# Kernel optimization log

Hardware: AMD Instinct MI355X
Metric: run time of the kernel (lower is better)

## Reference

```python
import jax, jax.numpy as jnp
import numpy as np

B, T, I, H, C, L, N_AHEAD = 64, 512, 64, 512, 512, 2, 24


def _lstm_layer(x, w_ih, w_hh, b_ih, b_hh):
    """PyTorch-convention LSTM layer. x: [B,T,in]. Returns (outputs [B,T,H], hT, cT)."""
    bsz = x.shape[0]
    hdim = w_hh.shape[1]
    bias = b_ih + b_hh

    def step(carry, xt):
        h, c = carry
        g = xt @ w_ih.T + h @ w_hh.T + bias  # [B, 4H], gate order i,f,g,o
        i, f, gg, o = jnp.split(g, 4, axis=-1)
        c = jax.nn.sigmoid(f) * c + jax.nn.sigmoid(i) * jnp.tanh(gg)
        h = jax.nn.sigmoid(o) * jnp.tanh(c)
        return (h, c), h

    init = (jnp.zeros((bsz, hdim), x.dtype), jnp.zeros((bsz, hdim), x.dtype))
    (hT, cT), hs = jax.lax.scan(step, init, jnp.swapaxes(x, 0, 1))
    return jnp.swapaxes(hs, 0, 1), hT, cT


def setup_inputs() -> dict:
    key = jax.random.key(0)
    ks = jax.random.split(key, 16)
    s = 0.04  # ~ 1/sqrt(H) init scale
    d = {
        "x": jax.random.normal(ks[0], (B, T, I), jnp.float32),
        "w_ih0": jax.random.normal(ks[1], (4 * H, I), jnp.float32) * s,
        "w_hh0": jax.random.normal(ks[2], (4 * H, H), jnp.float32) * s,
        "b_ih0": jax.random.normal(ks[3], (4 * H,), jnp.float32) * s,
        "b_hh0": jax.random.normal(ks[4], (4 * H,), jnp.float32) * s,
        "w_ih1": jax.random.normal(ks[5], (4 * H, H), jnp.float32) * s,
        "w_hh1": jax.random.normal(ks[6], (4 * H, H), jnp.float32) * s,
        "b_ih1": jax.random.normal(ks[7], (4 * H,), jnp.float32) * s,
        "b_hh1": jax.random.normal(ks[8], (4 * H,), jnp.float32) * s,
        "w_ih_dec": jax.random.normal(ks[9], (4 * H, C), jnp.float32) * s,
        "w_hh_dec": jax.random.normal(ks[10], (4 * H, H), jnp.float32) * s,
        "b_ih_dec": jax.random.normal(ks[11], (4 * H,), jnp.float32) * s,
        "b_hh_dec": jax.random.normal(ks[12], (4 * H,), jnp.float32) * s,
        "w_fc": jax.random.normal(ks[13], (C, H), jnp.float32) * s,
        "b_fc": jax.random.normal(ks[14], (C,), jnp.float32) * s,
    }
    return d


def reference(x, w_ih0, w_hh0, b_ih0, b_hh0, w_ih1, w_hh1, b_ih1, b_hh1,
              w_ih_dec, w_hh_dec, b_ih_dec, b_hh_dec, w_fc, b_fc):
    # ---- encoder: 2-layer LSTM, batch_first ----
    h0_out, _, _ = _lstm_layer(x, w_ih0, w_hh0, b_ih0, b_hh0)
    enc, hT, cT = _lstm_layer(h0_out, w_ih1, w_hh1, b_ih1, b_hh1)  # enc: [B,T,H]

    bsz = x.shape[0]
    dec_bias = b_ih_dec + b_hh_dec
    dec_in0 = jnp.zeros((bsz, C), x.dtype)

    def dec_step(carry, _):
        h, c, dec_in = carry
        aw = jax.nn.softmax(jnp.einsum('bth,bh->bt', enc, h), axis=1)  # [B,T]
        ctx = jnp.einsum('bt,bth->bh', aw, enc)                         # [B,H]
        xi = dec_in + ctx                                               # requires C == H
        g = xi @ w_ih_dec.T + h @ w_hh_dec.T + dec_bias
        i, f, gg, o = jnp.split(g, 4, axis=-1)
        c = jax.nn.sigmoid(f) * c + jax.nn.sigmoid(i) * jnp.tanh(gg)
        h = jax.nn.sigmoid(o) * jnp.tanh(c)
        pred = h @ w_fc.T + b_fc                                        # [B,C]
        return (h, c, pred), pred

    _, preds = jax.lax.scan(dec_step, (hT, cT, dec_in0), None, length=N_AHEAD)
    return jnp.swapaxes(preds, 0, 1)  # [B, n_ahead, C]
```

## Files before the change

### kernel.cpp

```cpp
#include <hip/hip_runtime.h>

#define BATCH  64
#define TT     512
#define IDIM   64
#define HDIM   512
#define NAHEAD 24
#define HB     (HDIM * BATCH)

#define WIH0_OFF   0
#define WHH0_OFF   512
#define WIH1_OFF   4608
#define WHH1_OFF   8704
#define SCR_OFF    12800
#define GL_OFF     30208
#define BIAS_OFF   31232
#define ENC_SMEM_FLOATS 31248
#define ENC_SMEM_BYTES  (ENC_SMEM_FLOATS * 4)

typedef float v2f __attribute__((ext_vector_type(2)));

__device__ __forceinline__ float4 ld4(const float* p) {
  return *reinterpret_cast<const float4*>(p);
}
__device__ __forceinline__ float sigm(float x) { return 1.0f / (1.0f + expf(-x)); }

__device__ __forceinline__ void flag_barrier(unsigned* flags, unsigned* release,
                                             unsigned epoch, int bid) {
  asm volatile("s_waitcnt vmcnt(0)" ::: "memory");
  __syncthreads();
  if (threadIdx.x == 0)
    __hip_atomic_store(&flags[(size_t)bid * 16], epoch,
                       __ATOMIC_RELAXED, __HIP_MEMORY_SCOPE_AGENT);
  asm volatile("" ::: "memory");
  if (bid == 0 && threadIdx.x < 64) {
    const int l = threadIdx.x;
    for (;;) {
      bool ok = true;
#pragma unroll
      for (int i = 0; i < 4; ++i) {
        unsigned v = __hip_atomic_load(&flags[(size_t)(l * 4 + i) * 16],
                                       __ATOMIC_RELAXED, __HIP_MEMORY_SCOPE_AGENT);
        ok &= (v >= epoch);
      }
      if (__all(ok)) break;
      __builtin_amdgcn_s_sleep(1);
    }
    if (threadIdx.x == 0)
      __hip_atomic_store(release, epoch, __ATOMIC_RELAXED,
                         __HIP_MEMORY_SCOPE_AGENT);
  }
  if (threadIdx.x == 0) {
    while (__hip_atomic_load(release, __ATOMIC_RELAXED,
                             __HIP_MEMORY_SCOPE_AGENT) < epoch)
      __builtin_amdgcn_s_sleep(1);
  }
  __syncthreads();
  asm volatile("" ::: "memory");
}

#define STG8(dst, base, off0)                                          \
  _Pragma("unroll") for (int i = 0; i < 8; ++i) {                      \
    dst[i].x = (base)[((off0) + i) * BATCH];                           \
    dst[i].y = (base)[((off0) + i) * BATCH + 32];                      \
  }

#define BURN_S(sarr, C0)                                                      \
  do {                                                                        \
    _Pragma("unroll") for (int c = 0; c < 8; c += 4) {                        \
      if (t < TT) {                                                           \
        _Pragma("unroll") for (int d = 0; d < 8; ++d) {                       \
          float4 w = ld4(&smem[WHH0_OFF + d * HDIM + ks * 16 + (C0) + c]);    \
          a0[d] += sarr[c]*w.x + sarr[c+1]*w.y + sarr[c+2]*w.z + sarr[c+3]*w.w;\
        }                                                                     \
      }                                                                       \
      if (t >= 1) {                                                           \
        _Pragma("unroll") for (int d = 0; d < 8; ++d) {                       \
          float4 w = ld4(&smem[WIH1_OFF + d * HDIM + ks * 16 + (C0) + c]);    \
          a1[d] += sarr[c]*w.x + sarr[c+1]*w.y + sarr[c+2]*w.z + sarr[c+3]*w.w;\
        }                                                                     \
      }                                                                       \
    }                                                                         \
  } while (0)

#define BURN_E(earr, C0)                                                      \
  do {                                                                        \
    if (t >= 1) {                                                             \
      _Pragma("unroll") for (int c = 0; c < 8; c += 4) {                      \
        _Pragma("unroll") for (int d = 0; d < 8; ++d) {                       \
          float4 w = ld4(&smem[WHH1_OFF + d * HDIM + ks * 16 + (C0) + c]);    \
          a1[d] += earr[c]*w.x + earr[c+1]*w.y + earr[c+2]*w.z + earr[c+3]*w.w;\
        }                                                                     \
      }                                                                       \
    }                                                                         \
  } while (0)

__global__ __launch_bounds__(1024, 4)
void encoder_coop(const float* __restrict__ xT,
                  const float* __restrict__ w_ih0, const float* __restrict__ w_hh0,
                  const float* __restrict__ b_ih0, const float* __restrict__ b_hh0,
                  const float* __restrict__ w_ih1, const float* __restrict__ w_hh1,
                  const float* __restrict__ b_ih1, const float* __restrict__ b_hh1,
                  float* __restrict__ seq0,
                  float* __restrict__ enc,
                  float* __restrict__ cst1,
                  unsigned* flags, unsigned* release)
{
  extern __shared__ float smem[];
  const int tid  = threadIdx.x;
  const int bid  = blockIdx.x;
  const int j0   = bid * 2;
  const int lane = tid & 63;
  const int wv   = tid >> 6;
  const int bp   = tid & 31;
  const int ks   = tid >> 5;

  for (int idx = tid; idx < 8 * IDIM; idx += 1024) {
    int d = idx >> 6, k = idx & 63;
    size_t r = (size_t)((d >> 1) * HDIM + j0 + (d & 1));
    smem[WIH0_OFF + idx] = w_ih0[r * IDIM + k];
  }
  for (int idx = tid; idx < 8 * HDIM; idx += 1024) {
    int d = idx >> 9, k = idx & 511;
    size_t r = (size_t)((d >> 1) * HDIM + j0 + (d & 1));
    smem[WHH0_OFF + idx] = w_hh0[r * HDIM + k];
    smem[WIH1_OFF + idx] = w_ih1[r * HDIM + k];
    smem[WHH1_OFF + idx] = w_hh1[r * HDIM + k];
  }
  if (tid < 16) {
    int d = tid & 7;
    size_t r = (size_t)((d >> 1) * HDIM + j0 + (d & 1));
    smem[BIAS_OFF + tid] = (tid < 8) ? (b_ih0[r] + b_hh0[r])
                                     : (b_ih1[r] + b_hh1[r]);
  }
  __syncthreads();

  float c0 = 0.f;
  float c1 = 0.f;

  for (int t = 0; t <= TT; ++t) {
    const float* sp = seq0 + (size_t)t * HB + (size_t)(ks * 16) * BATCH + bp;
    const float* ep = enc + (size_t)(t >= 1 ? t - 1 : 0) * HB
                          + (size_t)(ks * 16) * BATCH + bp;

    v2f sA[8], sB[8], eA[8], eB[8];
    v2f xv[4];

    STG8(sA, sp, 0);
    STG8(sB, sp, 8);
    if (t < TT && ks < 16) {
      const float* xp = xT + (size_t)t * IDIM * BATCH
                           + (size_t)(ks * 4) * BATCH + bp;
#pragma unroll
      for (int i = 0; i < 4; ++i) {
        xv[i].x = xp[i * BATCH];
        xv[i].y = xp[i * BATCH + 32];
      }
    }

    v2f a0[8], a1[8];
#pragma unroll
    for (int d = 0; d < 8; ++d) { a0[d] = 0.f; a1[d] = 0.f; }

    if (t < TT && ks < 16) {
#pragma unroll
      for (int d = 0; d < 8; ++d) {
        float4 w = ld4(&smem[WIH0_OFF + d * IDIM + ks * 4]);
        a0[d] += xv[0]*w.x + xv[1]*w.y + xv[2]*w.z + xv[3]*w.w;
      }
    }

    BURN_S(sA, 0);
    if (t >= 1) STG8(eA, ep, 0);
    BURN_S(sB, 8);
    if (t >= 1) STG8(eB, ep, 8);
    BURN_E(eA, 0);
    BURN_E(eB, 8);

#pragma unroll
    for (int d = 0; d < 8; ++d) {
      float m0x = a0[d].x + __shfl_xor(a0[d].x, 32);
      float m0y = a0[d].y + __shfl_xor(a0[d].y, 32);
      smem[SCR_OFF + (d * 64 + lane) * 17 + wv] = (lane >= 32) ? m0y : m0x;
      float m1x = a1[d].x + __shfl_xor(a1[d].x, 32);
      float m1y = a1[d].y + __shfl_xor(a1[d].y, 32);
      smem[SCR_OFF + ((8 + d) * 64 + lane) * 17 + wv] = (lane >= 32) ? m1y : m1x;
    }
    __syncthreads();

    {
      const int dd = tid >> 6, bb = tid & 63;
      float s = 0.f;
#pragma unroll
      for (int i = 0; i < 16; ++i) s += smem[SCR_OFF + (dd * 64 + bb) * 17 + i];
      smem[GL_OFF + dd * 64 + bb] = s + smem[BIAS_OFF + dd];
    }
    __syncthreads();

    if (tid < 256) {
      const int bb = tid & 63, u = tid >> 6;
      if (u < 2) {
        if (t < TT) {
          const int cl = u;
          float gi = smem[GL_OFF + (0 + cl) * 64 + bb];
          float gf = smem[GL_OFF + (2 + cl) * 64 + bb];
          float gg = smem[GL_OFF + (4 + cl) * 64 + bb];
          float go = smem[GL_OFF + (6 + cl) * 64 + bb];
          float cn = sigm(gf) * c0 + sigm(gi) * tanhf(gg);
          float hn = sigm(go) * tanhf(cn);
          c0 = cn;
          __hip_atomic_store(
              &seq0[(size_t)(t + 1) * HB + (size_t)(j0 + cl) * BATCH + bb],
              hn, __ATOMIC_RELAXED, __HIP_MEMORY_SCOPE_AGENT);
        }
      } else {
        if (t >= 1) {
          const int cl = u - 2;
          float gi = smem[GL_OFF + (8 + 0 + cl) * 64 + bb];
          float gf = smem[GL_OFF + (8 + 2 + cl) * 64 + bb];
          float gg = smem[GL_OFF + (8 + 4 + cl) * 64 + bb];
          float go = smem[GL_OFF + (8 + 6 + cl) * 64 + bb];
          float cn = sigm(gf) * c1 + sigm(gi) * tanhf(gg);
          float hn = sigm(go) * tanhf(cn);
          c1 = cn;
          __hip_atomic_store(
              &enc[(size_t)t * HB + (size_t)(j0 + cl) * BATCH + bb],
              hn, __ATOMIC_RELAXED, __HIP_MEMORY_SCOPE_AGENT);
        }
      }
    }

    if (t < TT) flag_barrier(flags, release, (unsigned)(t + 1), bid);
  }

  if (tid >= 128 && tid < 256)
    cst1[(size_t)(j0 + ((tid >> 6) - 2)) * BATCH + (tid & 63)] = c1;
}

template <int DIN0>
__device__ __forceinline__ void cell_tile2(
    int j0, const float* __restrict__ in0,
    const float* __restrict__ h_in,
    const float* __restrict__ w_ih,
    const float* __restrict__ w_hh,
    const float* __restrict__ b_ih, const float* __restrict__ b_hh,
    float* __restrict__ c_state,
    float* __restrict__ h_out,
    float* __restrict__ sm)
{
  const int tid = threadIdx.x;
  const int b  = tid & 63;
  const int ks = tid >> 6;
  constexpr int K  = DIN0 + HDIM;
  constexpr int KS = K / 16;
  const int k0 = ks * KS, k1 = k0 + KS;
  const int a0 = (k0 < DIN0) ? k0 : DIN0;
  const int a1 = (k1 < DIN0) ? k1 : DIN0;
  const int c0 = (k0 > DIN0) ? k0 - DIN0 : 0;
  const int c1 = (k1 > DIN0) ? k1 - DIN0 : 0;

  const float* wi = w_ih + (size_t)j0 * DIN0;
  const float* wh = w_hh + (size_t)j0 * HDIM;

  float acc[8] = {0.f, 0.f, 0.f, 0.f, 0.f, 0.f, 0.f, 0.f};

#pragma unroll 2
  for (int k = a0; k < a1; k += 4) {
    float x0 = in0[(k + 0) * BATCH + b];
    float x1 = in0[(k + 1) * BATCH + b];
    float x2 = in0[(k + 2) * BATCH + b];
    float x3 = in0[(k + 3) * BATCH + b];
#pragma unroll
    for (int d = 0; d < 8; ++d) {
      float4 w = ld4(wi + (size_t)((d >> 1) * HDIM + (d & 1)) * DIN0 + k);
      acc[d] += x0 * w.x + x1 * w.y + x2 * w.z + x3 * w.w;
    }
  }
#pragma unroll 2
  for (int k = c0; k < c1; k += 4) {
    float h0 = h_in[(k + 0) * BATCH + b];
    float h1 = h_in[(k + 1) * BATCH + b];
    float h2 = h_in[(k + 2) * BATCH + b];
    float h3 = h_in[(k + 3) * BATCH + b];
#pragma unroll
    for (int d = 0; d < 8; ++d) {
      float4 w = ld4(wh + (size_t)((d >> 1) * HDIM + (d & 1)) * HDIM + k);
      acc[d] += h0 * w.x + h1 * w.y + h2 * w.z + h3 * w.w;
    }
  }

  float* gl = sm + 8 * 64 * 17;
#pragma unroll
  for (int d = 0; d < 8; ++d) sm[(d * 64 + b) * 17 + ks] = acc[d];
  __syncthreads();

  if (tid < 512) {
    const int dd = tid >> 6, bb = tid & 63;
    float s = 0.f;
#pragma unroll
    for (int i = 0; i < 16; ++i) s += sm[(dd * 64 + bb) * 17 + i];
    const int r = (dd >> 1) * HDIM + j0 + (dd & 1);
    gl[dd * 64 + bb] = s + b_ih[r] + b_hh[r];
  }
  __syncthreads();

  if (tid < 128) {
    const int bb = tid & 63, cl = tid >> 6;
    const int jc = j0 + cl;
    float gi = gl[(0 + cl) * 64 + bb];
    float gf = gl[(2 + cl) * 64 + bb];
    float gg = gl[(4 + cl) * 64 + bb];
    float go = gl[(6 + cl) * 64 + bb];
    float cold = c_state[(size_t)jc * BATCH + bb];
    float cn = sigm(gf) * cold + sigm(gi) * tanhf(gg);
    float hn = sigm(go) * tanhf(cn);
    c_state[(size_t)jc * BATCH + bb] = cn;
    h_out[(size_t)jc * BATCH + bb] = hn;
  }
  __syncthreads();
}

__global__ __launch_bounds__(1024, 1)
void lstm_step(int t,
               const float* __restrict__ xT,
               const float* __restrict__ w_ih0, const float* __restrict__ w_hh0,
               const float* __restrict__ b_ih0, const float* __restrict__ b_hh0,
               const float* __restrict__ w_ih1, const float* __restrict__ w_hh1,
               const float* __restrict__ b_ih1, const float* __restrict__ b_hh1,
               float* __restrict__ seq0, float* __restrict__ enc,
               float* __restrict__ cst0, float* __restrict__ cst1)
{
  __shared__ float sm[8 * 64 * 17 + 8 * 64];
  const int j0 = blockIdx.x * 2;
  if (t < TT)
    cell_tile2<IDIM>(j0, xT + (size_t)t * IDIM * BATCH,
                     seq0 + (size_t)t * HB,
                     w_ih0, w_hh0, b_ih0, b_hh0,
                     cst0, seq0 + (size_t)(t + 1) * HB, sm);
  if (t >= 1)
    cell_tile2<HDIM>(j0, seq0 + (size_t)t * HB,
                     enc + (size_t)(t - 1) * HB,
                     w_ih1, w_hh1, b_ih1, b_hh1,
                     cst1, enc + (size_t)t * HB, sm);
}

__global__ __launch_bounds__(1024, 1)
void dec_gates(const float* __restrict__ xi, const float* __restrict__ h_cur,
               const float* __restrict__ w_ih, const float* __restrict__ w_hh,
               const float* __restrict__ b_ih, const float* __restrict__ b_hh,
               float* __restrict__ cst, float* __restrict__ h_out)
{
  __shared__ float sm[8 * 64 * 17 + 8 * 64];
  cell_tile2<HDIM>(blockIdx.x * 2, xi, h_cur, w_ih, w_hh, b_ih, b_hh,
                   cst, h_out, sm);
}

__global__ __launch_bounds__(512, 2)
void attn_scores(const float* __restrict__ enc,
                 const float* __restrict__ h_cur,
                 float* __restrict__ scores)
{
  __shared__ float red[2][8][64];
  const int tid = threadIdx.x;
  const int b  = tid & 63;
  const int ks = tid >> 6;
  const int t0 = blockIdx.x * 2;
  const float* e0 = enc + (size_t)(t0 + 1) * HB + ks * 64 * BATCH;
  const float* e1 = e0 + HB;
  const float* hr = h_cur + ks * 64 * BATCH;
  float a0 = 0.f, a1 = 0.f;
#pragma unroll 4
  for (int k = 0; k < 64; ++k) {
    float hv = hr[k * BATCH + b];
    a0 += hv * e0[k * BATCH + b];
    a1 += hv * e1[k * BATCH + b];
  }
  red[0][ks][b] = a0;
  red[1][ks][b] = a1;
  __syncthreads();
  if (tid < 128) {
    int tl = tid >> 6;
    float s = 0.f;
#pragma unroll
    for (int i = 0; i < 8; ++i) s += red[tl][i][b];
    scores[(size_t)(t0 + tl) * BATCH + b] = s;
  }
}

__global__ __launch_bounds__(512, 2)
void attn_ctx(const float* __restrict__ enc,
              const float* __restrict__ scores,
              const float* __restrict__ h_cur,
              const float* __restrict__ w_fc, const float* __restrict__ b_fc,
              float* __restrict__ xi,
              float* __restrict__ out,
              int s)
{
  __shared__ float red[8][2][64];
  __shared__ float mz[2][64];
  __shared__ float ctxv[2][64];
  const int tid = threadIdx.x;
  const int b  = tid & 63;
  const int ts = tid >> 6;
  const int hc0 = blockIdx.x * 2;

  float m = -1e30f;
  for (int t = ts * 64; t < ts * 64 + 64; ++t)
    m = fmaxf(m, scores[(size_t)t * BATCH + b]);
  red[ts][0][b] = m;
  __syncthreads();
  if (tid < 64) {
    float mm = red[0][0][b];
#pragma unroll
    for (int i = 1; i < 8; ++i) mm = fmaxf(mm, red[i][0][b]);
    mz[0][b] = mm;
  }
  __syncthreads();
  m = mz[0][b];
  float z = 0.f;
  for (int t = ts * 64; t < ts * 64 + 64; ++t)
    z += expf(scores[(size_t)t * BATCH + b] - m);
  red[ts][1][b] = z;
  __syncthreads();
  if (tid < 64) {
    float zz = 0.f;
#pragma unroll
    for (int i = 0; i < 8; ++i) zz += red[i][1][b];
    mz[1][b] = 1.f / zz;
  }
  __syncthreads();
  const float rZ = mz[1][b];

  float a0 = 0.f, a1 = 0.f;
  const float* eb = enc + HB + (size_t)hc0 * BATCH + b;
  for (int t = ts * 64; t < ts * 64 + 64; ++t) {
    float p = expf(scores[(size_t)t * BATCH + b] - m) * rZ;
    a0 += p * eb[(size_t)t * HB];
    a1 += p * eb[(size_t)t * HB + BATCH];
  }
  __syncthreads();
  red[ts][0][b] = a0;
  red[ts][1][b] = a1;
  __syncthreads();
  if (tid < 128) {
    int cl = tid >> 6;
    float c = 0.f;
#pragma unroll
    for (int i = 0; i < 8; ++i) c += red[i][cl][b];
    ctxv[cl][b] = c;
  }

  float p0 = 0.f, p1 = 0.f;
  if (s >= 1) {
    const float* w0 = w_fc + (size_t)hc0 * HDIM + ts * 64;
    const float* w1 = w0 + HDIM;
    const float* hr = h_cur + ts * 64 * BATCH;
#pragma unroll 2
    for (int k = 0; k < 64; k += 4) {
      float4 wa = ld4(w0 + k), wb = ld4(w1 + k);
      float h0 = hr[(k + 0) * BATCH + b], h1 = hr[(k + 1) * BATCH + b];
      float h2 = hr[(k + 2) * BATCH + b], h3 = hr[(k + 3) * BATCH + b];
      p0 += wa.x * h0 + wa.y * h1 + wa.z * h2 + wa.w * h3;
      p1 += wb.x * h0 + wb.y * h1 + wb.z * h2 + wb.w * h3;
    }
  }
  __syncthreads();
  red[ts][0][b] = p0;
  red[ts][1][b] = p1;
  __syncthreads();
  if (tid < 128) {
    int cl = tid >> 6;
    int cc = hc0 + cl;
    float pred = 0.f;
    if (s >= 1) {
#pragma unroll
      for (int i = 0; i < 8; ++i) pred += red[i][cl][b];
      pred += b_fc[cc];
      out[((size_t)b * NAHEAD + (s - 1)) * HDIM + cc] = pred;
    }
    xi[(size_t)cc * BATCH + b] = ctxv[cl][b] + pred;
  }
}

__global__ __launch_bounds__(512, 2)
void fc_out(const float* __restrict__ h, const float* __restrict__ w_fc,
            const float* __restrict__ b_fc, float* __restrict__ out, int srow)
{
  __shared__ float red[8][2][64];
  const int tid = threadIdx.x;
  const int b  = tid & 63;
  const int ks = tid >> 6;
  const int cc0 = blockIdx.x * 2;
  const float* w0 = w_fc + (size_t)cc0 * HDIM + ks * 64;
  const float* w1 = w0 + HDIM;
  const float* hr = h + ks * 64 * BATCH;
  float p0 = 0.f, p1 = 0.f;
#pragma unroll 2
  for (int k = 0; k < 64; k += 4) {
    float4 wa = ld4(w0 + k), wb = ld4(w1 + k);
    float h0 = hr[(k + 0) * BATCH + b], h1 = hr[(k + 1) * BATCH + b];
    float h2 = hr[(k + 2) * BATCH + b], h3 = hr[(k + 3) * BATCH + b];
    p0 += wa.x * h0 + wa.y * h1 + wa.z * h2 + wa.w * h3;
    p1 += wb.x * h0 + wb.y * h1 + wb.z * h2 + wb.w * h3;
  }
  red[ks][0][b] = p0;
  red[ks][1][b] = p1;
  __syncthreads();
  if (tid < 128) {
    int cl = tid >> 6;
    int cc = cc0 + cl;
    float p = 0.f;
#pragma unroll
    for (int i = 0; i < 8; ++i) p += red[i][cl][b];
    out[((size_t)b * NAHEAD + srow) * HDIM + cc] = p + b_fc[cc];
  }
}

__global__ __launch_bounds__(256)
void transpose_x(const float* __restrict__ x, float* __restrict__ xT)
{
  __shared__ float tile[64][65];
  const int t = blockIdx.x;
  const int lane = threadIdx.x & 63;
  const int w    = threadIdx.x >> 6;
#pragma unroll
  for (int ii = 0; ii < 16; ++ii) {
    int b = w * 16 + ii;
    tile[b][lane] = x[((size_t)b * TT + t) * IDIM + lane];
  }
  __syncthreads();
#pragma unroll
  for (int ii = 0; ii < 16; ++ii) {
    int i = w * 16 + ii;
    xT[((size_t)t * IDIM + i) * BATCH + lane] = tile[lane][i];
  }
}

extern "C" void kernel_launch(void* const* d_in, const int* in_sizes, int n_in,
                              void* d_out, int out_size, void* d_ws, size_t ws_size,
                              hipStream_t stream) {
  const float* x     = (const float*)d_in[0];
  const float* w_ih0 = (const float*)d_in[1];
  const float* w_hh0 = (const float*)d_in[2];
  const float* b_ih0 = (const float*)d_in[3];
  const float* b_hh0 = (const float*)d_in[4];
  const float* w_ih1 = (const float*)d_in[5];
  const float* w_hh1 = (const float*)d_in[6];
  const float* b_ih1 = (const float*)d_in[7];
  const float* b_hh1 = (const float*)d_in[8];
  const float* w_ihd = (const float*)d_in[9];
  const float* w_hhd = (const float*)d_in[10];
  const float* b_ihd = (const float*)d_in[11];
  const float* b_hhd = (const float*)d_in[12];
  const float* w_fc  = (const float*)d_in[13];
  const float* b_fc  = (const float*)d_in[14];
  float* out = (float*)d_out;

  char* ws = (char*)d_ws;
  size_t off = 0;
  auto alloc = [&](size_t bytes) -> void* {
    void* p = ws + off;
    off += (bytes + 255) & ~(size_t)255;
    return p;
  };

  float* cst0 = (float*)alloc((size_t)HB * 4);
  float* cst1 = (float*)alloc((size_t)HB * 4);
  float* seq0 = (float*)alloc((size_t)(TT + 1) * HB * 4);
  float* enc  = (float*)alloc((size_t)(TT + 1) * HB * 4);
  float* xT   = (float*)alloc((size_t)TT * IDIM * BATCH * 4);
  float* scores = (float*)alloc((size_t)TT * BATCH * 4);
  float* xi     = (float*)alloc((size_t)HB * 4);
  float* hdec   = (float*)alloc((size_t)2 * HB * 4);
  unsigned* flags   = (unsigned*)alloc(256 * 16 * 4);
  unsigned* release = (unsigned*)alloc(256);
  (void)ws_size; (void)in_sizes; (void)n_in; (void)out_size;

  hipMemsetAsync(cst0, 0, (size_t)HB * 4 * 2, stream);
  hipMemsetAsync(seq0, 0, (size_t)HB * 4, stream);
  hipMemsetAsync(enc,  0, (size_t)HB * 4, stream);
  hipMemsetAsync(flags, 0, 256 * 16 * 4, stream);
  hipMemsetAsync(release, 0, 256, stream);

  transpose_x<<<TT, 256, 0, stream>>>(x, xT);

  static bool attr_set = false;
  if (!attr_set) {
    hipFuncSetAttribute(reinterpret_cast<const void*>(encoder_coop),
                        hipFuncAttributeMaxDynamicSharedMemorySize,
                        ENC_SMEM_BYTES);
    attr_set = true;
  }
  void* args[] = {
    (void*)&xT,
    (void*)&w_ih0, (void*)&w_hh0, (void*)&b_ih0, (void*)&b_hh0,
    (void*)&w_ih1, (void*)&w_hh1, (void*)&b_ih1, (void*)&b_hh1,
    (void*)&seq0, (void*)&enc, (void*)&cst1, (void*)&flags, (void*)&release
  };
  hipError_t cerr = hipLaunchCooperativeKernel(
      reinterpret_cast<void*>(encoder_coop), dim3(256), dim3(1024),
      args, (unsigned)ENC_SMEM_BYTES, stream);
  if (cerr != hipSuccess) {
    for (int t = 0; t <= TT; ++t) {
      lstm_step<<<256, 1024, 0, stream>>>(
          t, xT, w_ih0, w_hh0, b_ih0, b_hh0,
          w_ih1, w_hh1, b_ih1, b_hh1, seq0, enc, cst0, cst1);
    }
  }

  const float* h_cur = enc + (size_t)TT * HB;
  for (int s = 0; s < NAHEAD; ++s) {
    attn_scores<<<256, 512, 0, stream>>>(enc, h_cur, scores);
    attn_ctx<<<256, 512, 0, stream>>>(enc, scores, h_cur, w_fc, b_fc,
                                      xi, out, s);
    float* h_nxt = hdec + (size_t)(s & 1) * HB;
    dec_gates<<<256, 1024, 0, stream>>>(xi, h_cur, w_ihd, w_hhd,
                                        b_ihd, b_hhd, cst1, h_nxt);
    h_cur = h_nxt;
  }
  fc_out<<<256, 512, 0, stream>>>(h_cur, w_fc, b_fc, out, NAHEAD - 1);
}
```

Before: 7.396 ms.

## Fuse decoder loop into a persistent cooperative kernel with flag barriers

Replaces the 24-step decoder's roughly 73 separate kernel launches (scores, context, gates, fc) with one cooperative persistent kernel. Each block keeps its slice of the decoder weights in shared memory and steps through the phases using grid-wide flag barriers. This removes per-step launch overhead and the repeated reloading of decoder weights. In exchange it adds three grid barriers per step, uses atomic loads for cross-block data, and keeps the old multi-kernel path as a fallback if the cooperative launch fails.

```diff
diff --git a/kernel.cpp b/kernel.cpp
--- a/kernel.cpp
+++ b/kernel.cpp
@@ -17,12 +17,30 @@
 #define ENC_SMEM_FLOATS 31248
 #define ENC_SMEM_BYTES  (ENC_SMEM_FLOATS * 4)
 
+#define DW_IH    0
+#define DW_HH    4096
+#define DSCR     8192
+#define DGL      16896
+#define DBIAS    17408
+#define DRED     17424
+#define DMZ      19472
+#define DCTX     19600
+#define DEC_SMEM_FLOATS 19728
+#define DEC_SMEM_BYTES  (DEC_SMEM_FLOATS * 4)
+
 typedef float v2f __attribute__((ext_vector_type(2)));
 
 __device__ __forceinline__ float4 ld4(const float* p) {
   return *reinterpret_cast<const float4*>(p);
 }
 __device__ __forceinline__ float sigm(float x) { return 1.0f / (1.0f + expf(-x)); }
+
+__device__ __forceinline__ float AL(const float* p) {
+  return __hip_atomic_load(p, __ATOMIC_RELAXED, __HIP_MEMORY_SCOPE_AGENT);
+}
+__device__ __forceinline__ void AS(float* p, float v) {
+  __hip_atomic_store(p, v, __ATOMIC_RELAXED, __HIP_MEMORY_SCOPE_AGENT);
+}
 
 __device__ __forceinline__ void flag_barrier(unsigned* flags, unsigned* release,
                                              unsigned epoch, int bid) {
@@ -208,9 +226,7 @@
           float cn = sigm(gf) * c0 + sigm(gi) * tanhf(gg);
           float hn = sigm(go) * tanhf(cn);
           c0 = cn;
-          __hip_atomic_store(
-              &seq0[(size_t)(t + 1) * HB + (size_t)(j0 + cl) * BATCH + bb],
-              hn, __ATOMIC_RELAXED, __HIP_MEMORY_SCOPE_AGENT);
+          AS(&seq0[(size_t)(t + 1) * HB + (size_t)(j0 + cl) * BATCH + bb], hn);
         }
       } else {
         if (t >= 1) {
@@ -222,9 +238,7 @@
           float cn = sigm(gf) * c1 + sigm(gi) * tanhf(gg);
           float hn = sigm(go) * tanhf(cn);
           c1 = cn;
-          __hip_atomic_store(
-              &enc[(size_t)t * HB + (size_t)(j0 + cl) * BATCH + bb],
-              hn, __ATOMIC_RELAXED, __HIP_MEMORY_SCOPE_AGENT);
+          AS(&enc[(size_t)t * HB + (size_t)(j0 + cl) * BATCH + bb], hn);
         }
       }
     }
@@ -234,6 +248,234 @@
 
   if (tid >= 128 && tid < 256)
     cst1[(size_t)(j0 + ((tid >> 6) - 2)) * BATCH + (tid & 63)] = c1;
+}
+
+__global__ __launch_bounds__(1024, 4)
+void decoder_coop(const float* __restrict__ enc,
+                  const float* __restrict__ w_ihd, const float* __restrict__ w_hhd,
+                  const float* __restrict__ b_ihd, const float* __restrict__ b_hhd,
+                  const float* __restrict__ w_fc, const float* __restrict__ b_fc,
+                  const float* __restrict__ cst1_in,
+                  float* __restrict__ scores, float* __restrict__ xi,
+                  float* __restrict__ hdec, float* __restrict__ out,
+                  unsigned* flags, unsigned* release)
+{
+  extern __shared__ float sm[];
+  const int tid = threadIdx.x;
+  const int bid = blockIdx.x;
+  const int j0  = bid * 2;
+  const int b   = tid & 63;
+
+  for (int idx = tid; idx < 8 * HDIM; idx += 1024) {
+    int d = idx >> 9, k = idx & 511;
+    size_t r = (size_t)((d >> 1) * HDIM + j0 + (d & 1));
+    sm[DW_IH + idx] = w_ihd[r * HDIM + k];
+    sm[DW_HH + idx] = w_hhd[r * HDIM + k];
+  }
+  if (tid < 8) {
+    size_t r = (size_t)((tid >> 1) * HDIM + j0 + (tid & 1));
+    sm[DBIAS + tid] = b_ihd[r] + b_hhd[r];
+  }
+  __syncthreads();
+
+  float c = 0.f;
+  if (tid < 128)
+    c = cst1_in[(size_t)(j0 + (tid >> 6)) * BATCH + (tid & 63)];
+
+  const float* h_cur = enc + (size_t)TT * HB;
+  unsigned ep = 0;
+
+  for (int s = 0; s < NAHEAD; ++s) {
+    {
+      const int tl = tid >> 9;
+      const int k8 = (tid >> 6) & 7;
+      const int t  = bid * 2 + tl;
+      const float* e  = enc + (size_t)(t + 1) * HB + (size_t)(k8 * 64) * BATCH + b;
+      const float* hr = h_cur + (size_t)(k8 * 64) * BATCH + b;
+      float a = 0.f;
+#pragma unroll 4
+      for (int k = 0; k < 64; ++k)
+        a += AL(hr + k * BATCH) * e[(size_t)k * BATCH];
+      sm[DRED + (tl * 8 + k8) * 64 + b] = a;
+      __syncthreads();
+      if (tid < 128) {
+        const int tl2 = tid >> 6;
+        float s8 = 0.f;
+#pragma unroll
+        for (int i = 0; i < 8; ++i) s8 += sm[DRED + (tl2 * 8 + i) * 64 + b];
+        AS(&scores[(size_t)(bid * 2 + tl2) * BATCH + b], s8);
+      }
+    }
+    flag_barrier(flags, release, ++ep, bid);
+
+    {
+      const int ts = tid >> 6;
+      float sc[32];
+#pragma unroll
+      for (int i = 0; i < 32; ++i)
+        sc[i] = AL(&scores[(size_t)(ts * 32 + i) * BATCH + b]);
+      float m = -1e30f;
+#pragma unroll
+      for (int i = 0; i < 32; ++i) m = fmaxf(m, sc[i]);
+      sm[DRED + ts * 64 + b] = m;
+      __syncthreads();
+      if (tid < 64) {
+        float mm = sm[DRED + b];
+#pragma unroll
+        for (int i = 1; i < 16; ++i) mm = fmaxf(mm, sm[DRED + i * 64 + b]);
+        sm[DMZ + b] = mm;
+      }
+      __syncthreads();
+      m = sm[DMZ + b];
+      float z = 0.f;
+#pragma unroll
+      for (int i = 0; i < 32; ++i) z += expf(sc[i] - m);
+      sm[DRED + (16 + ts) * 64 + b] = z;
+      __syncthreads();
+      if (tid < 64) {
+        float zz = 0.f;
+#pragma unroll
+        for (int i = 0; i < 16; ++i) zz += sm[DRED + (16 + i) * 64 + b];
+        sm[DMZ + 64 + b] = 1.f / zz;
+      }
+      __syncthreads();
+      const float rZ = sm[DMZ + 64 + b];
+
+      float a0 = 0.f, a1 = 0.f;
+      const float* eb = enc + HB + (size_t)j0 * BATCH + b;
+      for (int i = 0; i < 32; ++i) {
+        int t = ts * 32 + i;
+        float p = expf(sc[i] - m) * rZ;
+        a0 += p * eb[(size_t)t * HB];
+        a1 += p * eb[(size_t)t * HB + BATCH];
+      }
+      __syncthreads();
+      sm[DRED + ts * 64 + b] = a0;
+      sm[DRED + (16 + ts) * 64 + b] = a1;
+      __syncthreads();
+      if (tid < 128) {
+        const int cl = tid >> 6;
+        float cs = 0.f;
+#pragma unroll
+        for (int i = 0; i < 16; ++i) cs += sm[DRED + (cl * 16 + i) * 64 + b];
+        sm[DCTX + cl * 64 + b] = cs;
+      }
+
+      float p0 = 0.f, p1 = 0.f;
+      if (s >= 1) {
+        const float* w0 = w_fc + (size_t)j0 * HDIM + ts * 32;
+        const float* w1 = w0 + HDIM;
+        const float* hr = h_cur + (size_t)(ts * 32) * BATCH + b;
+#pragma unroll 2
+        for (int k = 0; k < 32; k += 4) {
+          float4 wa = ld4(w0 + k), wb = ld4(w1 + k);
+          float h0 = AL(hr + (k + 0) * BATCH), h1 = AL(hr + (k + 1) * BATCH);
+          float h2 = AL(hr + (k + 2) * BATCH), h3 = AL(hr + (k + 3) * BATCH);
+          p0 += wa.x*h0 + wa.y*h1 + wa.z*h2 + wa.w*h3;
+          p1 += wb.x*h0 + wb.y*h1 + wb.z*h2 + wb.w*h3;
+        }
+      }
+      __syncthreads();
+      sm[DRED + ts * 64 + b] = p0;
+      sm[DRED + (16 + ts) * 64 + b] = p1;
+      __syncthreads();
+      if (tid < 128) {
+        const int cl = tid >> 6;
+        const int cc = j0 + cl;
+        float pred = 0.f;
+        if (s >= 1) {
+#pragma unroll
+          for (int i = 0; i < 16; ++i) pred += sm[DRED + (cl * 16 + i) * 64 + b];
+          pred += b_fc[cc];
+          out[((size_t)b * NAHEAD + (s - 1)) * HDIM + cc] = pred;
+        }
+        AS(&xi[(size_t)cc * BATCH + b], sm[DCTX + cl * 64 + b] + pred);
+      }
+    }
+    flag_barrier(flags, release, ++ep, bid);
+
+    {
+      const int ks = tid >> 6;
+      float acc[8] = {0.f,0.f,0.f,0.f,0.f,0.f,0.f,0.f};
+      if (ks < 8) {
+        const float* ip = xi + (size_t)(ks * 64) * BATCH + b;
+#pragma unroll 2
+        for (int k = 0; k < 64; k += 4) {
+          float x0 = AL(ip + (k + 0) * BATCH), x1 = AL(ip + (k + 1) * BATCH);
+          float x2 = AL(ip + (k + 2) * BATCH), x3 = AL(ip + (k + 3) * BATCH);
+#pragma unroll
+          for (int d = 0; d < 8; ++d) {
+            float4 w = ld4(&sm[DW_IH + d * HDIM + ks * 64 + k]);
+            acc[d] += x0*w.x + x1*w.y + x2*w.z + x3*w.w;
+          }
+        }
+      } else {
+        const float* hp = h_cur + (size_t)((ks - 8) * 64) * BATCH + b;
+#pragma unroll 2
+        for (int k = 0; k < 64; k += 4) {
+          float h0 = AL(hp + (k + 0) * BATCH), h1 = AL(hp + (k + 1) * BATCH);
+          float h2 = AL(hp + (k + 2) * BATCH), h3 = AL(hp + (k + 3) * BATCH);
+#pragma unroll
+          for (int d = 0; d < 8; ++d) {
+            float4 w = ld4(&sm[DW_HH + d * HDIM + (ks - 8) * 64 + k]);
+            acc[d] += h0*w.x + h1*w.y + h2*w.z + h3*w.w;
+          }
+        }
+      }
+#pragma unroll
+      for (int d = 0; d < 8; ++d) sm[DSCR + (d * 64 + b) * 17 + ks] = acc[d];
+      __syncthreads();
+      if (tid < 512) {
+        const int dd = tid >> 6, bb = tid & 63;
+        float s16 = 0.f;
+#pragma unroll
+        for (int i = 0; i < 16; ++i) s16 += sm[DSCR + (dd * 64 + bb) * 17 + i];
+        sm[DGL + dd * 64 + bb] = s16 + sm[DBIAS + dd];
+      }
+      __syncthreads();
+      if (tid < 128) {
+        const int bb = tid & 63, cl = tid >> 6;
+        float gi = sm[DGL + (0 + cl) * 64 + bb];
+        float gf = sm[DGL + (2 + cl) * 64 + bb];
+        float gg = sm[DGL + (4 + cl) * 64 + bb];
+        float go = sm[DGL + (6 + cl) * 64 + bb];
+        float cn = sigm(gf) * c + sigm(gi) * tanhf(gg);
+        float hn = sigm(go) * tanhf(cn);
+        c = cn;
+        AS(&hdec[(size_t)(s & 1) * HB + (size_t)(j0 + cl) * BATCH + bb], hn);
+      }
+    }
+    h_cur = hdec + (size_t)(s & 1) * HB;
+    flag_barrier(flags, release, ++ep, bid);
+  }
+
+  {
+    const int ts = tid >> 6;
+    float p0 = 0.f, p1 = 0.f;
+    const float* w0 = w_fc + (size_t)j0 * HDIM + ts * 32;
+    const float* w1 = w0 + HDIM;
+    const float* hr = h_cur + (size_t)(ts * 32) * BATCH + b;
+#pragma unroll 2
+    for (int k = 0; k < 32; k += 4) {
+      float4 wa = ld4(w0 + k), wb = ld4(w1 + k);
+      float h0 = AL(hr + (k + 0) * BATCH), h1 = AL(hr + (k + 1) * BATCH);
+      float h2 = AL(hr + (k + 2) * BATCH), h3 = AL(hr + (k + 3) * BATCH);
+      p0 += wa.x*h0 + wa.y*h1 + wa.z*h2 + wa.w*h3;
+      p1 += wb.x*h0 + wb.y*h1 + wb.z*h2 + wb.w*h3;
+    }
+    __syncthreads();
+    sm[DRED + ts * 64 + b] = p0;
+    sm[DRED + (16 + ts) * 64 + b] = p1;
+    __syncthreads();
+    if (tid < 128) {
+      const int cl = tid >> 6;
+      const int cc = j0 + cl;
+      float p = 0.f;
+#pragma unroll
+      for (int i = 0; i < 16; ++i) p += sm[DRED + (cl * 16 + i) * 64 + b];
+      out[((size_t)b * NAHEAD + (NAHEAD - 1)) * HDIM + cc] = p + b_fc[cc];
+    }
+  }
 }
 
 template <int DIN0>
@@ -571,8 +813,10 @@
   float* scores = (float*)alloc((size_t)TT * BATCH * 4);
   float* xi     = (float*)alloc((size_t)HB * 4);
   float* hdec   = (float*)alloc((size_t)2 * HB * 4);
-  unsigned* flags   = (unsigned*)alloc(256 * 16 * 4);
-  unsigned* release = (unsigned*)alloc(256);
+  unsigned* flags    = (unsigned*)alloc(256 * 16 * 4);
+  unsigned* release  = (unsigned*)alloc(256);
+  unsigned* flags2   = (unsigned*)alloc(256 * 16 * 4);
+  unsigned* release2 = (unsigned*)alloc(256);
   (void)ws_size; (void)in_sizes; (void)n_in; (void)out_size;
 
   hipMemsetAsync(cst0, 0, (size_t)HB * 4 * 2, stream);
@@ -580,6 +824,8 @@
   hipMemsetAsync(enc,  0, (size_t)HB * 4, stream);
   hipMemsetAsync(flags, 0, 256 * 16 * 4, stream);
   hipMemsetAsync(release, 0, 256, stream);
+  hipMemsetAsync(flags2, 0, 256 * 16 * 4, stream);
+  hipMemsetAsync(release2, 0, 256, stream);
 
   transpose_x<<<TT, 256, 0, stream>>>(x, xT);
 
@@ -588,8 +834,12 @@
     hipFuncSetAttribute(reinterpret_cast<const void*>(encoder_coop),
                         hipFuncAttributeMaxDynamicSharedMemorySize,
                         ENC_SMEM_BYTES);
+    hipFuncSetAttribute(reinterpret_cast<const void*>(decoder_coop),
+                        hipFuncAttributeMaxDynamicSharedMemorySize,
+                        DEC_SMEM_BYTES);
     attr_set = true;
   }
+
   void* args[] = {
     (void*)&xT,
     (void*)&w_ih0, (void*)&w_hh0, (void*)&b_ih0, (void*)&b_hh0,
@@ -607,15 +857,26 @@
     }
   }
 
-  const float* h_cur = enc + (size_t)TT * HB;
-  for (int s = 0; s < NAHEAD; ++s) {
-    attn_scores<<<256, 512, 0, stream>>>(enc, h_cur, scores);
-    attn_ctx<<<256, 512, 0, stream>>>(enc, scores, h_cur, w_fc, b_fc,
-                                      xi, out, s);
-    float* h_nxt = hdec + (size_t)(s & 1) * HB;
-    dec_gates<<<256, 1024, 0, stream>>>(xi, h_cur, w_ihd, w_hhd,
-                                        b_ihd, b_hhd, cst1, h_nxt);
-    h_cur = h_nxt;
-  }
-  fc_out<<<256, 512, 0, stream>>>(h_cur, w_fc, b_fc, out, NAHEAD - 1);
-}
+  void* dargs[] = {
+    (void*)&enc, (void*)&w_ihd, (void*)&w_hhd, (void*)&b_ihd, (void*)&b_hhd,
+    (void*)&w_fc, (void*)&b_fc, (void*)&cst1,
+    (void*)&scores, (void*)&xi, (void*)&hdec, (void*)&out,
+    (void*)&flags2, (void*)&release2
+  };
+  hipError_t derr = hipLaunchCooperativeKernel(
+      reinterpret_cast<void*>(decoder_coop), dim3(256), dim3(1024),
+      dargs, (unsigned)DEC_SMEM_BYTES, stream);
+  if (derr != hipSuccess) {
+    const float* h_cur = enc + (size_t)TT * HB;
+    for (int s = 0; s < NAHEAD; ++s) {
+      attn_scores<<<256, 512, 0, stream>>>(enc, h_cur, scores);
+      attn_ctx<<<256, 512, 0, stream>>>(enc, scores, h_cur, w_fc, b_fc,
+                                        xi, out, s);
+      float* h_nxt = hdec + (size_t)(s & 1) * HB;
+      dec_gates<<<256, 1024, 0, stream>>>(xi, h_cur, w_ihd, w_hhd,
+                                          b_ihd, b_hhd, cst1, h_nxt);
+      h_cur = h_nxt;
+    }
+    fc_out<<<256, 512, 0, stream>>>(h_cur, w_fc, b_fc, out, NAHEAD - 1);
+  }
+}
```

Result: slower. 7.937 ms (+7.3%).
